# Performance work log

Measured on AMD Instinct MI355X. Metric: run time of the kernel, lower is better.

The kernel has to match this reference:

```python
import jax, jax.numpy as jnp
import numpy as np

B, N, M, D = 4096, 50, 64, 64   # batch, fields_dim, embedding_dim, product_layer_dim
V = 100000                      # features_dim (vocab)
HIDDEN = [512, 256, 128]
BN_EPS = 1e-3


def setup_inputs() -> dict:
    key = jax.random.key(0)
    ks = jax.random.split(key, 32)
    inp = {
        "feature_value": jax.random.uniform(ks[0], (B, N), dtype=jnp.float32),
        "embedding_index": jax.random.randint(ks[1], (B, N), 0, V, dtype=jnp.int32),
        "emb_table": jax.random.uniform(ks[2], (V, M), dtype=jnp.float32, minval=-0.05, maxval=0.05),
        "linear_signals": jax.random.normal(ks[3], (D, N, M), dtype=jnp.float32) * 0.05,
        "theta": jax.random.normal(ks[4], (D, N), dtype=jnp.float32) * 0.05,
        "quad_w": jax.random.normal(ks[5], (D, M, M), dtype=jnp.float32) * 0.05,
    }
    in_dim = 3 * D  # concat(l_z, l_p_inner, l_p_outer)
    dims = [in_dim] + HIDDEN
    k = 6
    for i, (di, do) in enumerate(zip(dims[:-1], dims[1:])):
        inp[f"W{i}"] = jax.random.normal(ks[k], (di, do), dtype=jnp.float32) * (1.0 / np.sqrt(di)); k += 1
        inp[f"b{i}"] = jnp.zeros((do,), dtype=jnp.float32)
        inp[f"g{i}"] = jnp.ones((do,), dtype=jnp.float32)
        inp[f"be{i}"] = jnp.zeros((do,), dtype=jnp.float32)
        inp[f"m{i}"] = jnp.zeros((do,), dtype=jnp.float32)
        inp[f"v{i}"] = jnp.ones((do,), dtype=jnp.float32)
    inp["Wout"] = jax.random.normal(ks[k], (HIDDEN[-1], 1), dtype=jnp.float32) * (1.0 / np.sqrt(HIDDEN[-1]))
    inp["bout"] = jnp.zeros((1,), dtype=jnp.float32)
    return inp


def _pnn_forward(feature_value, embedding_index, emb_table, linear_signals, theta, quad_w,
                 dense_params, Wout, bout):
    # features: [b, n, m] = embedding lookup scaled per-field by feature_value
    feats = emb_table[embedding_index] * feature_value[:, :, None]
    # linear signal: 'bnm,dnm->bd'
    l_z = jnp.einsum('bnm,dnm->bd', feats, linear_signals)
    # ipnn branch: delta = 'dn,bnm->bdnm'; l_p = sum delta*delta over (n,m)
    # algebraic rewrite (same math): sum_n theta_dn^2 * (sum_m feats_bnm^2)
    l_p_in = jnp.einsum('bn,dn->bd', jnp.sum(feats * feats, axis=2), theta * theta)
    # opnn branch: p = outer(sum_feats, sum_feats); 'bmn,dmn->bd'
    s = jnp.sum(feats, axis=1)  # [b, m]
    l_p_out = jnp.einsum('bm,dmn,bn->bd', s, quad_w, s)
    x = jnp.concatenate([l_z, l_p_in, l_p_out], axis=1)  # [b, 3d]
    # MLP stack: Dense -> BatchNorm(inference) -> ReLU (dropout is identity at eval)
    for (W, b, g, be, mu, var) in dense_params:
        x = x @ W + b
        x = g * (x - mu) * jax.lax.rsqrt(var + BN_EPS) + be
        x = jax.nn.relu(x)
    return jax.nn.sigmoid(x @ Wout + bout)


def reference(feature_value, embedding_index, emb_table, linear_signals, theta, quad_w,
              W0, b0, g0, be0, m0, v0,
              W1, b1, g1, be1, m1, v1,
              W2, b2, g2, be2, m2, v2,
              Wout, bout):
    dense_params = [(W0, b0, g0, be0, m0, v0),
                    (W1, b1, g1, be1, m1, v1),
                    (W2, b2, g2, be2, m2, v2)]
    return _pnn_forward(feature_value, embedding_index, emb_table, linear_signals, theta,
                        quad_w, dense_params, Wout, bout)
```

## Files before the change

### kernel.cpp

```cpp
#include <hip/hip_runtime.h>
#include <hip/hip_bf16.h>
#include <math.h>

#define B 4096
#define NF 50
#define BN_EPS 1e-3f
#define ROWS 16

typedef float f32x4 __attribute__((ext_vector_type(4)));
typedef __bf16 bf16x8 __attribute__((ext_vector_type(8)));
#define MFMA __builtin_amdgcn_mfma_f32_16x16x32_bf16

__device__ __forceinline__ unsigned short f2b(float x) {
  unsigned u = __float_as_uint(x);
  return (unsigned short)((u + 0x7FFFu + ((u >> 16) & 1u)) >> 16);
}
__device__ __forceinline__ unsigned packbf(float a, float b) {
  return ((unsigned)f2b(b) << 16) | (unsigned)f2b(a);
}
__device__ __forceinline__ float bs2f(unsigned short u) {
  return __uint_as_float(((unsigned)u) << 16);
}

#define WS_LS  0
#define WS_QW  204800
#define WS_W0  466944
#define WS_W1  565248
#define WS_W2  696320

__global__ __launch_bounds__(256) void prep(
    const float* __restrict__ ls, const float* __restrict__ qw,
    const float* __restrict__ W0, const float* __restrict__ W1,
    const float* __restrict__ W2, unsigned short* __restrict__ ws)
{
  int tid = blockIdx.x * 256 + threadIdx.x;
  if (tid < 25600) {
    int o = tid * 8;
    float4 a = *(const float4*)(ls + o), b = *(const float4*)(ls + o + 4);
    int4 v = {(int)packbf(a.x, a.y), (int)packbf(a.z, a.w),
              (int)packbf(b.x, b.y), (int)packbf(b.z, b.w)};
    *(int4*)&ws[WS_LS + o] = v; return;
  }
  tid -= 25600;
  if (tid < 32768) {
    int o = tid * 8;
    float4 a = *(const float4*)(qw + o), b = *(const float4*)(qw + o + 4);
    int4 v = {(int)packbf(a.x, a.y), (int)packbf(a.z, a.w),
              (int)packbf(b.x, b.y), (int)packbf(b.z, b.w)};
    *(int4*)&ws[WS_QW + o] = v; return;
  }
  tid -= 32768;
  if (tid < 12288) {
    int n = tid / 24, k0 = (tid - n * 24) * 8;
    float f[8];
#pragma unroll
    for (int j = 0; j < 8; ++j) f[j] = W0[(k0 + j) * 512 + n];
    int4 v = {(int)packbf(f[0], f[1]), (int)packbf(f[2], f[3]),
              (int)packbf(f[4], f[5]), (int)packbf(f[6], f[7])};
    *(int4*)&ws[WS_W0 + n * 192 + k0] = v; return;
  }
  tid -= 12288;
  if (tid < 16384) {
    int n = tid >> 6, k0 = (tid & 63) * 8;
    float f[8];
#pragma unroll
    for (int j = 0; j < 8; ++j) f[j] = W1[(k0 + j) * 256 + n];
    int4 v = {(int)packbf(f[0], f[1]), (int)packbf(f[2], f[3]),
              (int)packbf(f[4], f[5]), (int)packbf(f[6], f[7])};
    *(int4*)&ws[WS_W1 + n * 512 + k0] = v; return;
  }
  tid -= 16384;
  if (tid < 4096) {
    int n = tid >> 5, k0 = (tid & 31) * 8;
    float f[8];
#pragma unroll
    for (int j = 0; j < 8; ++j) f[j] = W2[(k0 + j) * 128 + n];
    int4 v = {(int)packbf(f[0], f[1]), (int)packbf(f[2], f[3]),
              (int)packbf(f[4], f[5]), (int)packbf(f[6], f[7])};
    *(int4*)&ws[WS_W2 + n * 256 + k0] = v;
  }
}

__global__ __launch_bounds__(512, 4) void pnn_main(
    const float* __restrict__ fv, const int* __restrict__ idx,
    const float* __restrict__ emb, const float* __restrict__ theta,
    const unsigned short* __restrict__ ws,
    const float* __restrict__ b0p, const float* __restrict__ g0p,
    const float* __restrict__ be0p, const float* __restrict__ m0p,
    const float* __restrict__ v0p,
    const float* __restrict__ b1p, const float* __restrict__ g1p,
    const float* __restrict__ be1p, const float* __restrict__ m1p,
    const float* __restrict__ v1p,
    const float* __restrict__ b2p, const float* __restrict__ g2p,
    const float* __restrict__ be2p, const float* __restrict__ m2p,
    const float* __restrict__ v2p,
    const float* __restrict__ Wout, const float* __restrict__ boutp,
    float* __restrict__ out)
{
  __shared__ int   idx_s[ROWS * NF];
  __shared__ float fv_s[ROWS * NF];
  __shared__ float s_s[ROWS * 64];
  __shared__ float sq_s[ROWS * 64];
  __shared__ float red_s[4 * 256];
  __shared__ unsigned short x_s[ROWS * 200];
  __shared__ unsigned short h0_s[ROWS * 520];
  __shared__ unsigned short h1_s[ROWS * 264];
  __shared__ unsigned short h2_s[ROWS * 136];
  __shared__ unsigned short fbuf[2 * 2 * ROWS * 136];

  const unsigned short* lsb = ws + WS_LS;
  const unsigned short* qwb = ws + WS_QW;
  const unsigned short* w0t = ws + WS_W0;
  const unsigned short* w1t = ws + WS_W1;
  const unsigned short* w2t = ws + WS_W2;

  const int t  = threadIdx.x;
  const int w  = t >> 6;
  const int l  = t & 63;
  const int m16 = l & 15;
  const int qoff = (l >> 4) * 8;
  const int b0 = blockIdx.x * ROWS;
  const int bq = t >> 5;
  const int i2 = (t & 31) * 2;
  const int kh = w >> 2;
  const int d0 = (w & 3) * 16;

  for (int i = t; i < ROWS * NF; i += 512) {
    idx_s[i] = idx[b0 * NF + i];
    fv_s[i]  = fv[b0 * NF + i];
  }
  __syncthreads();

  float s0 = 0.f, s1 = 0.f;
  f32x4 az0 = {0.f, 0.f, 0.f, 0.f}, az1 = {0.f, 0.f, 0.f, 0.f};

  for (int c = 0; c < 13; ++c) {
    unsigned short* fb = fbuf + (c & 1) * 4352;
#pragma unroll
    for (int h = 0; h < 4; ++h) {
      int n = 4 * c + h;
      if (n < NF) {
        int iv = idx_s[bq * NF + n];
        float fvv = fv_s[bq * NF + n];
        float2 e = *(const float2*)(emb + (size_t)iv * 64 + i2);
        float p0 = fvv * e.x, p1 = fvv * e.y;
        *(unsigned*)&fb[(h >> 1) * 2176 + bq * 136 + (h & 1) * 64 + i2] = packbf(p0, p1);
        s0 += p0; s1 += p1;
        float q = p0 * p0 + p1 * p1;
        q += __shfl_xor(q, 16); q += __shfl_xor(q, 8); q += __shfl_xor(q, 4);
        q += __shfl_xor(q, 2);  q += __shfl_xor(q, 1);
        if ((t & 31) == 0) sq_s[bq * 64 + n] = q;
      }
    }
    __syncthreads();
    if (!(kh == 1 && c == 12)) {
      const unsigned short* fa = fb + kh * 2176;
      const unsigned short* lp = lsb + (d0 + m16) * 3200 + 256 * c + kh * 128 + qoff;
      int ar = m16 * 136 + qoff;
      bf16x8 bv0 = *(const bf16x8*)(lp);
      bf16x8 bv1 = *(const bf16x8*)(lp + 32);
      bf16x8 bv2 = *(const bf16x8*)(lp + 64);
      bf16x8 bv3 = *(const bf16x8*)(lp + 96);
      bf16x8 a0 = *(const bf16x8*)&fa[ar];
      bf16x8 a1 = *(const bf16x8*)&fa[ar + 32];
      bf16x8 a2 = *(const bf16x8*)&fa[ar + 64];
      bf16x8 a3 = *(const bf16x8*)&fa[ar + 96];
      az0 = MFMA(a0, bv0, az0, 0, 0, 0);
      az1 = MFMA(a1, bv1, az1, 0, 0, 0);
      az0 = MFMA(a2, bv2, az0, 0, 0, 0);
      az1 = MFMA(a3, bv3, az1, 0, 0, 0);
    }
  }
  { float2 sv; sv.x = s0; sv.y = s1; *(float2*)&s_s[bq * 64 + i2] = sv; }
  __syncthreads();

  {
    f32x4 cz;
#pragma unroll
    for (int r = 0; r < 4; ++r) cz[r] = az0[r] + az1[r];
    if (w >= 4) {
      int base = (w - 4) * 256;
#pragma unroll
      for (int r = 0; r < 4; ++r)
        red_s[base + ((l >> 4) * 4 + r) * 16 + m16] = cz[r];
    }
    __syncthreads();
    if (w < 4) {
      int base = w * 256;
#pragma unroll
      for (int r = 0; r < 4; ++r) {
        float v = cz[r] + red_s[base + ((l >> 4) * 4 + r) * 16 + m16];
        x_s[((l >> 4) * 4 + r) * 200 + w * 16 + m16] = f2b(v);
      }
    }
    int d = t & 63, g = t >> 6;
#pragma unroll
    for (int e = 0; e < 2; ++e) {
      int bb = g + 8 * e;
      float a = 0.f;
      for (int n = 0; n < NF; ++n) {
        float th = theta[d * NF + n];
        a += sq_s[bb * 64 + n] * (th * th);
      }
      x_s[bb * 200 + 64 + d] = f2b(a);
    }
  }
  __syncthreads();

  {
    f32x4 ap0 = {0.f, 0.f, 0.f, 0.f}, ap1 = {0.f, 0.f, 0.f, 0.f};
    for (int c = 0; c < 16; ++c) {
      unsigned short* fb = fbuf + (c & 1) * 4352;
#pragma unroll
      for (int h = 0; h < 4; ++h) {
        int mq = 4 * c + h;
        float pm = s_s[bq * 64 + mq];
        float p0 = pm * s_s[bq * 64 + i2];
        float p1 = pm * s_s[bq * 64 + i2 + 1];
        *(unsigned*)&fb[(h >> 1) * 2176 + bq * 136 + (h & 1) * 64 + i2] = packbf(p0, p1);
      }
      __syncthreads();
      {
        const unsigned short* fa = fb + kh * 2176;
        const unsigned short* qp = qwb + (d0 + m16) * 4096 + 256 * c + kh * 128 + qoff;
        int ar = m16 * 136 + qoff;
        bf16x8 bv0 = *(const bf16x8*)(qp);
        bf16x8 bv1 = *(const bf16x8*)(qp + 32);
        bf16x8 bv2 = *(const bf16x8*)(qp + 64);
        bf16x8 bv3 = *(const bf16x8*)(qp + 96);
        bf16x8 a0 = *(const bf16x8*)&fa[ar];
        bf16x8 a1 = *(const bf16x8*)&fa[ar + 32];
        bf16x8 a2 = *(const bf16x8*)&fa[ar + 64];
        bf16x8 a3 = *(const bf16x8*)&fa[ar + 96];
        ap0 = MFMA(a0, bv0, ap0, 0, 0, 0);
        ap1 = MFMA(a1, bv1, ap1, 0, 0, 0);
        ap0 = MFMA(a2, bv2, ap0, 0, 0, 0);
        ap1 = MFMA(a3, bv3, ap1, 0, 0, 0);
      }
    }
    f32x4 cp;
#pragma unroll
    for (int r = 0; r < 4; ++r) cp[r] = ap0[r] + ap1[r];
    __syncthreads();
    if (w >= 4) {
      int base = (w - 4) * 256;
#pragma unroll
      for (int r = 0; r < 4; ++r)
        red_s[base + ((l >> 4) * 4 + r) * 16 + m16] = cp[r];
    }
    __syncthreads();
    if (w < 4) {
      int base = w * 256;
#pragma unroll
      for (int r = 0; r < 4; ++r) {
        float v = cp[r] + red_s[base + ((l >> 4) * 4 + r) * 16 + m16];
        x_s[((l >> 4) * 4 + r) * 200 + 128 + w * 16 + m16] = f2b(v);
      }
    }
  }
  __syncthreads();

  {
    int ar = m16 * 200 + qoff;
    bf16x8 xa[6];
#pragma unroll
    for (int kc = 0; kc < 6; ++kc) xa[kc] = *(const bf16x8*)&x_s[ar + kc * 32];
    for (int j = 0; j < 4; ++j) {
      int n0 = (w * 4 + j) * 16;
      const unsigned short* wp = w0t + (n0 + m16) * 192 + qoff;
      f32x4 ha = {0.f, 0.f, 0.f, 0.f}, hb = {0.f, 0.f, 0.f, 0.f};
#pragma unroll
      for (int kc = 0; kc < 6; ++kc) {
        bf16x8 bv = *(const bf16x8*)(wp + kc * 32);
        if (kc & 1) hb = MFMA(xa[kc], bv, hb, 0, 0, 0);
        else        ha = MFMA(xa[kc], bv, ha, 0, 0, 0);
      }
      int n = n0 + m16;
      float sc = g0p[n] * rsqrtf(v0p[n] + BN_EPS);
      float sh = be0p[n] + (b0p[n] - m0p[n]) * sc;
#pragma unroll
      for (int r = 0; r < 4; ++r) {
        float v = fmaxf((ha[r] + hb[r]) * sc + sh, 0.f);
        h0_s[((l >> 4) * 4 + r) * 520 + n] = f2b(v);
      }
    }
  }
  __syncthreads();

  for (int j = 0; j < 2; ++j) {
    int n0 = (w * 2 + j) * 16;
    const unsigned short* wp = w1t + (n0 + m16) * 512 + qoff;
    int ar = m16 * 520 + qoff;
    f32x4 ha = {0.f, 0.f, 0.f, 0.f}, hb = {0.f, 0.f, 0.f, 0.f};
#pragma unroll
    for (int kc = 0; kc < 16; ++kc) {
      bf16x8 av = *(const bf16x8*)&h0_s[ar + kc * 32];
      bf16x8 bv = *(const bf16x8*)(wp + kc * 32);
      if (kc & 1) hb = MFMA(av, bv, hb, 0, 0, 0);
      else        ha = MFMA(av, bv, ha, 0, 0, 0);
    }
    int n = n0 + m16;
    float sc = g1p[n] * rsqrtf(v1p[n] + BN_EPS);
    float sh = be1p[n] + (b1p[n] - m1p[n]) * sc;
#pragma unroll
    for (int r = 0; r < 4; ++r) {
      float v = fmaxf((ha[r] + hb[r]) * sc + sh, 0.f);
      h1_s[((l >> 4) * 4 + r) * 264 + n] = f2b(v);
    }
  }
  __syncthreads();

  {
    int n0 = w * 16;
    const unsigned short* wp = w2t + (n0 + m16) * 256 + qoff;
    int ar = m16 * 264 + qoff;
    f32x4 ha = {0.f, 0.f, 0.f, 0.f}, hb = {0.f, 0.f, 0.f, 0.f};
#pragma unroll
    for (int kc = 0; kc < 8; ++kc) {
      bf16x8 av = *(const bf16x8*)&h1_s[ar + kc * 32];
      bf16x8 bv = *(const bf16x8*)(wp + kc * 32);
      if (kc & 1) hb = MFMA(av, bv, hb, 0, 0, 0);
      else        ha = MFMA(av, bv, ha, 0, 0, 0);
    }
    int n = n0 + m16;
    float sc = g2p[n] * rsqrtf(v2p[n] + BN_EPS);
    float sh = be2p[n] + (b2p[n] - m2p[n]) * sc;
#pragma unroll
    for (int r = 0; r < 4; ++r) {
      float v = fmaxf((ha[r] + hb[r]) * sc + sh, 0.f);
      h2_s[((l >> 4) * 4 + r) * 136 + n] = f2b(v);
    }
  }
  __syncthreads();

  if (t < 128) {
    int bb = t >> 3, seg = t & 7;
    float a = 0.f;
#pragma unroll
    for (int j = 0; j < 16; ++j) {
      int k = seg * 16 + j;
      a += bs2f(h2_s[bb * 136 + k]) * Wout[k];
    }
    a += __shfl_xor(a, 4); a += __shfl_xor(a, 2); a += __shfl_xor(a, 1);
    if (seg == 0) out[b0 + bb] = 1.f / (1.f + expf(-(a + boutp[0])));
  }
}

extern "C" void kernel_launch(void* const* d_in, const int* in_sizes, int n_in,
                              void* d_out, int out_size, void* d_ws, size_t ws_size,
                              hipStream_t stream)
{
  (void)in_sizes; (void)n_in; (void)out_size; (void)ws_size;
  unsigned short* ws = (unsigned short*)d_ws;

  prep<<<356, 256, 0, stream>>>(
      (const float*)d_in[3], (const float*)d_in[5], (const float*)d_in[6],
      (const float*)d_in[12], (const float*)d_in[18], ws);

  pnn_main<<<B / ROWS, 512, 0, stream>>>(
      (const float*)d_in[0], (const int*)d_in[1], (const float*)d_in[2],
      (const float*)d_in[4], ws,
      (const float*)d_in[7],  (const float*)d_in[8],  (const float*)d_in[9],
      (const float*)d_in[10], (const float*)d_in[11],
      (const float*)d_in[13], (const float*)d_in[14], (const float*)d_in[15],
      (const float*)d_in[16], (const float*)d_in[17],
      (const float*)d_in[19], (const float*)d_in[20], (const float*)d_in[21],
      (const float*)d_in[22], (const float*)d_in[23],
      (const float*)d_in[24], (const float*)d_in[25],
      (float*)d_out);
}
```

Measured before the change: 207.5 us.

## Halve rows per block, drop K-split reduction, tile weight transpose via LDS

The main kernel now handles 8 batch rows per 256-thread block, so there are twice as many blocks. Each wave owns a full 16-wide output slice over the whole K range, which removes the cross-wave split-K reduction through shared memory and its extra barriers. Theta squared is cached in LDS, and the prep kernel transposes weights through 64x64 shared tiles with coalesced reads instead of strided gathers. The cost is that half of every 16-row MFMA tile is wasted on duplicate rows, and weight loads from L2 are repeated per block for twice as many blocks.

```diff
diff --git a/kernel.cpp b/kernel.cpp
--- a/kernel.cpp
+++ b/kernel.cpp
@@ -5,7 +5,7 @@
 #define B 4096
 #define NF 50
 #define BN_EPS 1e-3f
-#define ROWS 16
+#define ROWS 8
 
 typedef float f32x4 __attribute__((ext_vector_type(4)));
 typedef __bf16 bf16x8 __attribute__((ext_vector_type(8)));
@@ -33,55 +33,47 @@
     const float* __restrict__ W0, const float* __restrict__ W1,
     const float* __restrict__ W2, unsigned short* __restrict__ ws)
 {
-  int tid = blockIdx.x * 256 + threadIdx.x;
-  if (tid < 25600) {
-    int o = tid * 8;
-    float4 a = *(const float4*)(ls + o), b = *(const float4*)(ls + o + 4);
+  int bid = blockIdx.x, t = threadIdx.x;
+  if (bid < 228) {
+    int o = (bid * 256 + t) * 8;
+    const float* src = (o < 204800) ? (ls + o) : (qw + (o - 204800));
+    float4 a = *(const float4*)src, b = *(const float4*)(src + 4);
     int4 v = {(int)packbf(a.x, a.y), (int)packbf(a.z, a.w),
               (int)packbf(b.x, b.y), (int)packbf(b.z, b.w)};
-    *(int4*)&ws[WS_LS + o] = v; return;
-  }
-  tid -= 25600;
-  if (tid < 32768) {
-    int o = tid * 8;
-    float4 a = *(const float4*)(qw + o), b = *(const float4*)(qw + o + 4);
-    int4 v = {(int)packbf(a.x, a.y), (int)packbf(a.z, a.w),
-              (int)packbf(b.x, b.y), (int)packbf(b.z, b.w)};
-    *(int4*)&ws[WS_QW + o] = v; return;
-  }
-  tid -= 32768;
-  if (tid < 12288) {
-    int n = tid / 24, k0 = (tid - n * 24) * 8;
-    float f[8];
-#pragma unroll
-    for (int j = 0; j < 8; ++j) f[j] = W0[(k0 + j) * 512 + n];
-    int4 v = {(int)packbf(f[0], f[1]), (int)packbf(f[2], f[3]),
-              (int)packbf(f[4], f[5]), (int)packbf(f[6], f[7])};
-    *(int4*)&ws[WS_W0 + n * 192 + k0] = v; return;
-  }
-  tid -= 12288;
-  if (tid < 16384) {
-    int n = tid >> 6, k0 = (tid & 63) * 8;
-    float f[8];
-#pragma unroll
-    for (int j = 0; j < 8; ++j) f[j] = W1[(k0 + j) * 256 + n];
-    int4 v = {(int)packbf(f[0], f[1]), (int)packbf(f[2], f[3]),
-              (int)packbf(f[4], f[5]), (int)packbf(f[6], f[7])};
-    *(int4*)&ws[WS_W1 + n * 512 + k0] = v; return;
-  }
-  tid -= 16384;
-  if (tid < 4096) {
-    int n = tid >> 5, k0 = (tid & 31) * 8;
-    float f[8];
-#pragma unroll
-    for (int j = 0; j < 8; ++j) f[j] = W2[(k0 + j) * 128 + n];
-    int4 v = {(int)packbf(f[0], f[1]), (int)packbf(f[2], f[3]),
-              (int)packbf(f[4], f[5]), (int)packbf(f[6], f[7])};
-    *(int4*)&ws[WS_W2 + n * 256 + k0] = v;
-  }
-}
-
-__global__ __launch_bounds__(512, 4) void pnn_main(
+    *(int4*)&ws[o] = v;
+    return;
+  }
+  __shared__ unsigned short sh[64 * 72];
+  int id = bid - 228;
+  const float* W; int K, Ncols, kt, nt, wofs;
+  if (id < 24)      { W = W0; K = 192; Ncols = 512; kt = id >> 3; nt = id & 7;  wofs = WS_W0; }
+  else if (id < 56) { int j = id - 24; W = W1; K = 512; Ncols = 256; kt = j >> 2; nt = j & 3; wofs = WS_W1; }
+  else              { int j = id - 56; W = W2; K = 256; Ncols = 128; kt = j >> 1; nt = j & 1; wofs = WS_W2; }
+  int k0 = kt * 64, n0 = nt * 64;
+  {
+    int r = t >> 2, cs = (t & 3) * 16;
+    const float* src = W + (size_t)(k0 + r) * Ncols + n0 + cs;
+    float4 a = *(const float4*)src, b = *(const float4*)(src + 4);
+    float4 c = *(const float4*)(src + 8), d = *(const float4*)(src + 12);
+    unsigned short* dst = &sh[r * 72 + cs];
+    *(int4*)dst = int4{(int)packbf(a.x, a.y), (int)packbf(a.z, a.w),
+                       (int)packbf(b.x, b.y), (int)packbf(b.z, b.w)};
+    *(int4*)(dst + 8) = int4{(int)packbf(c.x, c.y), (int)packbf(c.z, c.w),
+                             (int)packbf(d.x, d.y), (int)packbf(d.z, d.w)};
+  }
+  __syncthreads();
+  {
+    int nr = t >> 2, ks = (t & 3) * 16;
+    unsigned short vbuf[16];
+#pragma unroll
+    for (int j = 0; j < 16; ++j) vbuf[j] = sh[(ks + j) * 72 + nr];
+    unsigned short* dst = &ws[wofs + (size_t)(n0 + nr) * K + k0 + ks];
+    *(int4*)dst = *(int4*)&vbuf[0];
+    *(int4*)(dst + 8) = *(int4*)&vbuf[8];
+  }
+}
+
+__global__ __launch_bounds__(256, 4) void pnn_main(
     const float* __restrict__ fv, const int* __restrict__ idx,
     const float* __restrict__ emb, const float* __restrict__ theta,
     const unsigned short* __restrict__ ws,
@@ -99,14 +91,14 @@
 {
   __shared__ int   idx_s[ROWS * NF];
   __shared__ float fv_s[ROWS * NF];
+  __shared__ float th2_s[64 * NF];
   __shared__ float s_s[ROWS * 64];
   __shared__ float sq_s[ROWS * 64];
-  __shared__ float red_s[4 * 256];
+  __shared__ unsigned short fbuf[2][ROWS * 264];
   __shared__ unsigned short x_s[ROWS * 200];
   __shared__ unsigned short h0_s[ROWS * 520];
   __shared__ unsigned short h1_s[ROWS * 264];
   __shared__ unsigned short h2_s[ROWS * 136];
-  __shared__ unsigned short fbuf[2 * 2 * ROWS * 136];
 
   const unsigned short* lsb = ws + WS_LS;
   const unsigned short* qwb = ws + WS_QW;
@@ -114,37 +106,39 @@
   const unsigned short* w1t = ws + WS_W1;
   const unsigned short* w2t = ws + WS_W2;
 
-  const int t  = threadIdx.x;
-  const int w  = t >> 6;
-  const int l  = t & 63;
-  const int m16 = l & 15;
+  const int t    = threadIdx.x;
+  const int w    = t >> 6;
+  const int l    = t & 63;
+  const int m16  = l & 15;
   const int qoff = (l >> 4) * 8;
-  const int b0 = blockIdx.x * ROWS;
-  const int bq = t >> 5;
-  const int i2 = (t & 31) * 2;
-  const int kh = w >> 2;
-  const int d0 = (w & 3) * 16;
-
-  for (int i = t; i < ROWS * NF; i += 512) {
+  const int d0   = w * 16;
+  const int b0   = blockIdx.x * ROWS;
+  const int bq   = t >> 5;
+  const int i2   = (t & 31) * 2;
+  const int arow = (m16 & 7) * 264 + qoff;
+
+  for (int i = t; i < ROWS * NF; i += 256) {
     idx_s[i] = idx[b0 * NF + i];
     fv_s[i]  = fv[b0 * NF + i];
   }
+  for (int i = t; i < 64 * NF; i += 256) { float v = theta[i]; th2_s[i] = v * v; }
   __syncthreads();
 
   float s0 = 0.f, s1 = 0.f;
   f32x4 az0 = {0.f, 0.f, 0.f, 0.f}, az1 = {0.f, 0.f, 0.f, 0.f};
 
   for (int c = 0; c < 13; ++c) {
-    unsigned short* fb = fbuf + (c & 1) * 4352;
+    unsigned short* fb = fbuf[c & 1];
+    int nfld = (c < 12) ? 4 : 2;
 #pragma unroll
     for (int h = 0; h < 4; ++h) {
-      int n = 4 * c + h;
-      if (n < NF) {
+      if (h < nfld) {
+        int n = 4 * c + h;
         int iv = idx_s[bq * NF + n];
         float fvv = fv_s[bq * NF + n];
         float2 e = *(const float2*)(emb + (size_t)iv * 64 + i2);
         float p0 = fvv * e.x, p1 = fvv * e.y;
-        *(unsigned*)&fb[(h >> 1) * 2176 + bq * 136 + (h & 1) * 64 + i2] = packbf(p0, p1);
+        *(unsigned*)&fb[bq * 264 + h * 64 + i2] = packbf(p0, p1);
         s0 += p0; s1 += p1;
         float q = p0 * p0 + p1 * p1;
         q += __shfl_xor(q, 16); q += __shfl_xor(q, 8); q += __shfl_xor(q, 4);
@@ -153,121 +147,77 @@
       }
     }
     __syncthreads();
-    if (!(kh == 1 && c == 12)) {
-      const unsigned short* fa = fb + kh * 2176;
-      const unsigned short* lp = lsb + (d0 + m16) * 3200 + 256 * c + kh * 128 + qoff;
-      int ar = m16 * 136 + qoff;
-      bf16x8 bv0 = *(const bf16x8*)(lp);
-      bf16x8 bv1 = *(const bf16x8*)(lp + 32);
-      bf16x8 bv2 = *(const bf16x8*)(lp + 64);
-      bf16x8 bv3 = *(const bf16x8*)(lp + 96);
-      bf16x8 a0 = *(const bf16x8*)&fa[ar];
-      bf16x8 a1 = *(const bf16x8*)&fa[ar + 32];
-      bf16x8 a2 = *(const bf16x8*)&fa[ar + 64];
-      bf16x8 a3 = *(const bf16x8*)&fa[ar + 96];
-      az0 = MFMA(a0, bv0, az0, 0, 0, 0);
-      az1 = MFMA(a1, bv1, az1, 0, 0, 0);
-      az0 = MFMA(a2, bv2, az0, 0, 0, 0);
-      az1 = MFMA(a3, bv3, az1, 0, 0, 0);
+    const unsigned short* lp = lsb + (size_t)(d0 + m16) * 3200 + c * 256 + qoff;
+    int nfr = nfld * 2;
+#pragma unroll 4
+    for (int kc = 0; kc < nfr; ++kc) {
+      bf16x8 av = *(const bf16x8*)&fb[arow + kc * 32];
+      bf16x8 bv = *(const bf16x8*)(lp + kc * 32);
+      if (kc & 1) az1 = MFMA(av, bv, az1, 0, 0, 0);
+      else        az0 = MFMA(av, bv, az0, 0, 0, 0);
     }
   }
   { float2 sv; sv.x = s0; sv.y = s1; *(float2*)&s_s[bq * 64 + i2] = sv; }
-  __syncthreads();
-
-  {
-    f32x4 cz;
-#pragma unroll
-    for (int r = 0; r < 4; ++r) cz[r] = az0[r] + az1[r];
-    if (w >= 4) {
-      int base = (w - 4) * 256;
-#pragma unroll
-      for (int r = 0; r < 4; ++r)
-        red_s[base + ((l >> 4) * 4 + r) * 16 + m16] = cz[r];
-    }
-    __syncthreads();
-    if (w < 4) {
-      int base = w * 256;
-#pragma unroll
-      for (int r = 0; r < 4; ++r) {
-        float v = cz[r] + red_s[base + ((l >> 4) * 4 + r) * 16 + m16];
-        x_s[((l >> 4) * 4 + r) * 200 + w * 16 + m16] = f2b(v);
-      }
-    }
+  if (l < 32) {
+#pragma unroll
+    for (int r = 0; r < 4; ++r) {
+      float v = az0[r] + az1[r];
+      x_s[((l >> 4) * 4 + r) * 200 + d0 + m16] = f2b(v);
+    }
+  }
+  {
     int d = t & 63, g = t >> 6;
-#pragma unroll
-    for (int e = 0; e < 2; ++e) {
-      int bb = g + 8 * e;
-      float a = 0.f;
-      for (int n = 0; n < NF; ++n) {
-        float th = theta[d * NF + n];
-        a += sq_s[bb * 64 + n] * (th * th);
-      }
-      x_s[bb * 200 + 64 + d] = f2b(a);
-    }
+    float a0 = 0.f, a1 = 0.f;
+    for (int n = 0; n < NF; ++n) {
+      float th2 = th2_s[d * NF + n];
+      a0 += sq_s[g * 64 + n] * th2;
+      a1 += sq_s[(g + 4) * 64 + n] * th2;
+    }
+    x_s[g * 200 + 64 + d]       = f2b(a0);
+    x_s[(g + 4) * 200 + 64 + d] = f2b(a1);
   }
   __syncthreads();
 
   {
     f32x4 ap0 = {0.f, 0.f, 0.f, 0.f}, ap1 = {0.f, 0.f, 0.f, 0.f};
     for (int c = 0; c < 16; ++c) {
-      unsigned short* fb = fbuf + (c & 1) * 4352;
+      unsigned short* fb = fbuf[c & 1];
 #pragma unroll
       for (int h = 0; h < 4; ++h) {
         int mq = 4 * c + h;
         float pm = s_s[bq * 64 + mq];
         float p0 = pm * s_s[bq * 64 + i2];
         float p1 = pm * s_s[bq * 64 + i2 + 1];
-        *(unsigned*)&fb[(h >> 1) * 2176 + bq * 136 + (h & 1) * 64 + i2] = packbf(p0, p1);
+        *(unsigned*)&fb[bq * 264 + h * 64 + i2] = packbf(p0, p1);
       }
       __syncthreads();
-      {
-        const unsigned short* fa = fb + kh * 2176;
-        const unsigned short* qp = qwb + (d0 + m16) * 4096 + 256 * c + kh * 128 + qoff;
-        int ar = m16 * 136 + qoff;
-        bf16x8 bv0 = *(const bf16x8*)(qp);
-        bf16x8 bv1 = *(const bf16x8*)(qp + 32);
-        bf16x8 bv2 = *(const bf16x8*)(qp + 64);
-        bf16x8 bv3 = *(const bf16x8*)(qp + 96);
-        bf16x8 a0 = *(const bf16x8*)&fa[ar];
-        bf16x8 a1 = *(const bf16x8*)&fa[ar + 32];
-        bf16x8 a2 = *(const bf16x8*)&fa[ar + 64];
-        bf16x8 a3 = *(const bf16x8*)&fa[ar + 96];
-        ap0 = MFMA(a0, bv0, ap0, 0, 0, 0);
-        ap1 = MFMA(a1, bv1, ap1, 0, 0, 0);
-        ap0 = MFMA(a2, bv2, ap0, 0, 0, 0);
-        ap1 = MFMA(a3, bv3, ap1, 0, 0, 0);
-      }
-    }
-    f32x4 cp;
-#pragma unroll
-    for (int r = 0; r < 4; ++r) cp[r] = ap0[r] + ap1[r];
-    __syncthreads();
-    if (w >= 4) {
-      int base = (w - 4) * 256;
-#pragma unroll
-      for (int r = 0; r < 4; ++r)
-        red_s[base + ((l >> 4) * 4 + r) * 16 + m16] = cp[r];
-    }
-    __syncthreads();
-    if (w < 4) {
-      int base = w * 256;
+      const unsigned short* qp = qwb + (size_t)(d0 + m16) * 4096 + c * 256 + qoff;
+#pragma unroll
+      for (int kc = 0; kc < 8; ++kc) {
+        bf16x8 av = *(const bf16x8*)&fb[arow + kc * 32];
+        bf16x8 bv = *(const bf16x8*)(qp + kc * 32);
+        if (kc & 1) ap1 = MFMA(av, bv, ap1, 0, 0, 0);
+        else        ap0 = MFMA(av, bv, ap0, 0, 0, 0);
+      }
+    }
+    if (l < 32) {
 #pragma unroll
       for (int r = 0; r < 4; ++r) {
-        float v = cp[r] + red_s[base + ((l >> 4) * 4 + r) * 16 + m16];
-        x_s[((l >> 4) * 4 + r) * 200 + 128 + w * 16 + m16] = f2b(v);
-      }
-    }
-  }
-  __syncthreads();
-
-  {
-    int ar = m16 * 200 + qoff;
+        float v = ap0[r] + ap1[r];
+        x_s[((l >> 4) * 4 + r) * 200 + 128 + d0 + m16] = f2b(v);
+      }
+    }
+  }
+  __syncthreads();
+
+  {
+    int ar = (m16 & 7) * 200 + qoff;
     bf16x8 xa[6];
 #pragma unroll
     for (int kc = 0; kc < 6; ++kc) xa[kc] = *(const bf16x8*)&x_s[ar + kc * 32];
-    for (int j = 0; j < 4; ++j) {
-      int n0 = (w * 4 + j) * 16;
-      const unsigned short* wp = w0t + (n0 + m16) * 192 + qoff;
+    for (int j = 0; j < 8; ++j) {
+      int n0 = (w * 8 + j) * 16;
+      const unsigned short* wp = w0t + (size_t)(n0 + m16) * 192 + qoff;
       f32x4 ha = {0.f, 0.f, 0.f, 0.f}, hb = {0.f, 0.f, 0.f, 0.f};
 #pragma unroll
       for (int kc = 0; kc < 6; ++kc) {
@@ -275,22 +225,24 @@
         if (kc & 1) hb = MFMA(xa[kc], bv, hb, 0, 0, 0);
         else        ha = MFMA(xa[kc], bv, ha, 0, 0, 0);
       }
-      int n = n0 + m16;
-      float sc = g0p[n] * rsqrtf(v0p[n] + BN_EPS);
-      float sh = be0p[n] + (b0p[n] - m0p[n]) * sc;
-#pragma unroll
-      for (int r = 0; r < 4; ++r) {
-        float v = fmaxf((ha[r] + hb[r]) * sc + sh, 0.f);
-        h0_s[((l >> 4) * 4 + r) * 520 + n] = f2b(v);
-      }
-    }
-  }
-  __syncthreads();
-
-  for (int j = 0; j < 2; ++j) {
-    int n0 = (w * 2 + j) * 16;
-    const unsigned short* wp = w1t + (n0 + m16) * 512 + qoff;
-    int ar = m16 * 520 + qoff;
+      if (l < 32) {
+        int n = n0 + m16;
+        float sc = g0p[n] * rsqrtf(v0p[n] + BN_EPS);
+        float sh = be0p[n] + (b0p[n] - m0p[n]) * sc;
+#pragma unroll
+        for (int r = 0; r < 4; ++r) {
+          float v = fmaxf((ha[r] + hb[r]) * sc + sh, 0.f);
+          h0_s[((l >> 4) * 4 + r) * 520 + n] = f2b(v);
+        }
+      }
+    }
+  }
+  __syncthreads();
+
+  for (int j = 0; j < 4; ++j) {
+    int n0 = (w * 4 + j) * 16;
+    const unsigned short* wp = w1t + (size_t)(n0 + m16) * 512 + qoff;
+    int ar = (m16 & 7) * 520 + qoff;
     f32x4 ha = {0.f, 0.f, 0.f, 0.f}, hb = {0.f, 0.f, 0.f, 0.f};
 #pragma unroll
     for (int kc = 0; kc < 16; ++kc) {
@@ -299,21 +251,23 @@
       if (kc & 1) hb = MFMA(av, bv, hb, 0, 0, 0);
       else        ha = MFMA(av, bv, ha, 0, 0, 0);
     }
-    int n = n0 + m16;
-    float sc = g1p[n] * rsqrtf(v1p[n] + BN_EPS);
-    float sh = be1p[n] + (b1p[n] - m1p[n]) * sc;
-#pragma unroll
-    for (int r = 0; r < 4; ++r) {
-      float v = fmaxf((ha[r] + hb[r]) * sc + sh, 0.f);
-      h1_s[((l >> 4) * 4 + r) * 264 + n] = f2b(v);
-    }
-  }
-  __syncthreads();
-
-  {
-    int n0 = w * 16;
-    const unsigned short* wp = w2t + (n0 + m16) * 256 + qoff;
-    int ar = m16 * 264 + qoff;
+    if (l < 32) {
+      int n = n0 + m16;
+      float sc = g1p[n] * rsqrtf(v1p[n] + BN_EPS);
+      float sh = be1p[n] + (b1p[n] - m1p[n]) * sc;
+#pragma unroll
+      for (int r = 0; r < 4; ++r) {
+        float v = fmaxf((ha[r] + hb[r]) * sc + sh, 0.f);
+        h1_s[((l >> 4) * 4 + r) * 264 + n] = f2b(v);
+      }
+    }
+  }
+  __syncthreads();
+
+  for (int j = 0; j < 2; ++j) {
+    int n0 = (w * 2 + j) * 16;
+    const unsigned short* wp = w2t + (size_t)(n0 + m16) * 256 + qoff;
+    int ar = (m16 & 7) * 264 + qoff;
     f32x4 ha = {0.f, 0.f, 0.f, 0.f}, hb = {0.f, 0.f, 0.f, 0.f};
 #pragma unroll
     for (int kc = 0; kc < 8; ++kc) {
@@ -322,18 +276,20 @@
       if (kc & 1) hb = MFMA(av, bv, hb, 0, 0, 0);
       else        ha = MFMA(av, bv, ha, 0, 0, 0);
     }
-    int n = n0 + m16;
-    float sc = g2p[n] * rsqrtf(v2p[n] + BN_EPS);
-    float sh = be2p[n] + (b2p[n] - m2p[n]) * sc;
-#pragma unroll
-    for (int r = 0; r < 4; ++r) {
-      float v = fmaxf((ha[r] + hb[r]) * sc + sh, 0.f);
-      h2_s[((l >> 4) * 4 + r) * 136 + n] = f2b(v);
-    }
-  }
-  __syncthreads();
-
-  if (t < 128) {
+    if (l < 32) {
+      int n = n0 + m16;
+      float sc = g2p[n] * rsqrtf(v2p[n] + BN_EPS);
+      float sh = be2p[n] + (b2p[n] - m2p[n]) * sc;
+#pragma unroll
+      for (int r = 0; r < 4; ++r) {
+        float v = fmaxf((ha[r] + hb[r]) * sc + sh, 0.f);
+        h2_s[((l >> 4) * 4 + r) * 136 + n] = f2b(v);
+      }
+    }
+  }
+  __syncthreads();
+
+  if (t < 64) {
     int bb = t >> 3, seg = t & 7;
     float a = 0.f;
 #pragma unroll
@@ -353,11 +309,11 @@
   (void)in_sizes; (void)n_in; (void)out_size; (void)ws_size;
   unsigned short* ws = (unsigned short*)d_ws;
 
-  prep<<<356, 256, 0, stream>>>(
+  prep<<<292, 256, 0, stream>>>(
       (const float*)d_in[3], (const float*)d_in[5], (const float*)d_in[6],
       (const float*)d_in[12], (const float*)d_in[18], ws);
 
-  pnn_main<<<B / ROWS, 512, 0, stream>>>(
+  pnn_main<<<B / ROWS, 256, 0, stream>>>(
       (const float*)d_in[0], (const int*)d_in[1], (const float*)d_in[2],
       (const float*)d_in[4], ws,
       (const float*)d_in[7],  (const float*)d_in[8],  (const float*)d_in[9],
```

New measurement: 227.1 us. 1.09x slower.
